# Kernel optimization log

Hardware: AMD Instinct MI355X
Metric: run time of the kernel (lower is better)

## Reference

```python
import jax, jax.numpy as jnp
import numpy as np

WS = 7          # window size
NUM_HEADS = 12

def _relative_position_index(ws):
    # Same construction as the torch module; pure numpy constants.
    coords = np.stack(np.meshgrid(np.arange(ws), np.arange(ws), indexing='ij'))  # [2, ws, ws]
    flat = coords.reshape(2, -1)                                                 # [2, N]
    rel = flat[:, :, None] - flat[:, None, :]                                    # [2, N, N]
    rel = rel.transpose(1, 2, 0).copy()                                          # [N, N, 2]
    rel[:, :, 0] += ws - 1
    rel[:, :, 1] += ws - 1
    rel[:, :, 0] *= 2 * ws - 1
    return rel.sum(-1)                                                           # [N, N] int

REL_IDX = jnp.asarray(_relative_position_index(WS))

def setup_inputs() -> dict:
    key = jax.random.key(0)
    ks = jax.random.split(key, 7)
    C, H = 384, NUM_HEADS
    B_, N = 2048, WS * WS
    return {
        "x": jax.random.normal(ks[0], (B_, N, C), jnp.float32),
        "mask": jax.random.normal(ks[1], (64, N, N), jnp.float32),
        "qkv_w": jax.random.normal(ks[2], (3 * C, C), jnp.float32) * 0.02,
        "qkv_b": jax.random.normal(ks[3], (3 * C,), jnp.float32) * 0.02,
        "proj_w": jax.random.normal(ks[4], (C, C), jnp.float32) * 0.02,
        "proj_b": jax.random.normal(ks[5], (C,), jnp.float32) * 0.02,
        "rpb_table": jax.random.normal(ks[6], ((2 * WS - 1) ** 2, H), jnp.float32) * 0.02,
    }

def reference(x, mask, qkv_w, qkv_b, proj_w, proj_b, rpb_table):
    B_, N, C = x.shape
    H = NUM_HEADS
    hd = C // H
    scale = hd ** (-0.5)

    qkv = x @ qkv_w.T + qkv_b                                   # [B_, N, 3C]
    qkv = qkv.reshape(B_, N, 3, H, hd).transpose(2, 0, 3, 1, 4)  # [3, B_, H, N, hd]
    q, k, v = qkv[0], qkv[1], qkv[2]

    attn = jnp.einsum('bhnd,bhmd->bhnm', q * scale, k)          # [B_, H, N, N]

    bias = rpb_table[REL_IDX]                                   # [N, N, H]
    attn = attn + bias.transpose(2, 0, 1)[None]                 # + [1, H, N, N]

    nw = mask.shape[0]
    attn = attn.reshape(B_ // nw, nw, H, N, N) + mask[None, :, None]
    attn = attn.reshape(B_, H, N, N)
    attn = jax.nn.softmax(attn, axis=-1)

    out = jnp.einsum('bhnm,bhmd->bhnd', attn, v)                # [B_, H, N, hd]
    out = out.transpose(0, 2, 1, 3).reshape(B_, N, C)
    return out @ proj_w.T + proj_b
```

## Files before the change

### kernel.cpp

```cpp
#include <hip/hip_runtime.h>
#include <stdint.h>
#include <stddef.h>

#define BWIN 2048
#define NTOK 49
#define CDIM 384
#define HNUM 12
#define HD   32
#define MTOT (BWIN * NTOK)
#define LOG2E 1.4426950408889634f
#define QSCALE ((float)(0.17677669529663687 * 1.4426950408889634))

typedef __attribute__((ext_vector_type(8))) short short8;
typedef __attribute__((ext_vector_type(4))) float floatx4;

__device__ __forceinline__ unsigned short f2bf(float f) {
    union { float f; unsigned u; } v; v.f = f;
    unsigned u = v.u;
    u = u + 0x7fffu + ((u >> 16) & 1u);
    return (unsigned short)(u >> 16);
}

__device__ __forceinline__ void gload16(const void* g, void* l) {
    __builtin_amdgcn_global_load_lds(
        (const __attribute__((address_space(1))) void*)g,
        (__attribute__((address_space(3))) void*)l, 16, 0, 0);
}

#define XBLK  18816
#define WQBLK 216
#define WPBLK 72
__global__ __launch_bounds__(256) void convert_kernel(
    const float* __restrict__ x, const float* __restrict__ wq,
    const float* __restrict__ wp, unsigned short* __restrict__ xbf,
    unsigned short* __restrict__ wqbf, unsigned short* __restrict__ wpbf)
{
    int bid = blockIdx.x;
    const float* src; unsigned short* dst; size_t base;
    if (bid < XBLK)              { src = x;  dst = xbf;  base = (size_t)bid * 2048; }
    else if (bid < XBLK + WQBLK) { src = wq; dst = wqbf; base = (size_t)(bid - XBLK) * 2048; }
    else                         { src = wp; dst = wpbf; base = (size_t)(bid - XBLK - WQBLK) * 2048; }
    const size_t i = base + (size_t)threadIdx.x * 8;
    float4 a = *(const float4*)(src + i);
    float4 b = *(const float4*)(src + i + 4);
    unsigned short o[8] = {f2bf(a.x), f2bf(a.y), f2bf(a.z), f2bf(a.w),
                           f2bf(b.x), f2bf(b.y), f2bf(b.z), f2bf(b.w)};
    *(uint4*)(dst + i) = *(uint4*)o;
}

__global__ __launch_bounds__(256) void bias_kernel(
    const float* __restrict__ mask, const float* __restrict__ rpb,
    float* __restrict__ cb)
{
    const int bm = blockIdx.x, h = blockIdx.y;
    const int tid = threadIdx.x;
    const int w = tid >> 6, lane = tid & 63;
    const int cg = lane & 15, rg = lane >> 4;
    const int rbase = 16 * w + (rg << 2);
    const float* mk = mask + (size_t)bm * (NTOK * NTOK);
    float o[16];
    #pragma unroll
    for (int j = 0; j < 4; ++j) {
        const int col = 16 * j + cg;
        const bool vc = col < NTOK;
        int yj = 0, xj = 0;
        if (vc) { yj = col / 7; xj = col - yj * 7; }
        #pragma unroll
        for (int r = 0; r < 4; ++r) {
            const int row = rbase + r;
            float v = -1e30f;
            if (vc && row < NTOK) {
                const int yi = row / 7, xi = row - yi * 7;
                const int rel = (yi - yj + 6) * 13 + (xi - xj + 6);
                v = (rpb[rel * HNUM + h] + mk[row * NTOK + col]) * LOG2E;
            }
            o[4 * j + r] = v;
        }
    }
    float* dst = cb + ((size_t)bm * HNUM + h) * 4096 + (size_t)tid * 16;
    #pragma unroll
    for (int j = 0; j < 4; ++j)
        *(float4*)(dst + 4 * j) = *(const float4*)(o + 4 * j);
}

__global__ __launch_bounds__(256) void qkv_kernel(
    const unsigned short* __restrict__ a, const unsigned short* __restrict__ b,
    const float* __restrict__ bias, unsigned short* __restrict__ outq)
{
    __shared__ __align__(16) unsigned short lA[3][128 * 32];
    __shared__ __align__(16) unsigned short lB[3][128 * 32];

    const int tid = threadIdx.x;
    const int lane = tid & 63, w = tid >> 6;

    const int bid = blockIdx.x;
    const int wg = (bid & 7) * 882 + (bid >> 3);
    const int tN = (wg % 9) * 128;
    const int tM = (wg / 9) * 128;

    const int X = (lane << 4) ^ (((lane >> 3) & 7) << 4);
    const int srow = (w << 5) + (X >> 6);
    const int scol = (X & 63) >> 1;
    const unsigned short* gA = a + (size_t)(tM + srow) * CDIM + scol;
    const unsigned short* gB = b + (size_t)(tN + srow) * CDIM + scol;

    const int wm = (w & 1) << 6, wn = (w >> 1) << 6;
    const int cg = lane & 15, rg = lane >> 4;

    floatx4 acc[4][4];
    #pragma unroll
    for (int i = 0; i < 4; ++i)
        #pragma unroll
        for (int j = 0; j < 4; ++j) acc[i][j] = (floatx4){0.f, 0.f, 0.f, 0.f};

    int offA[4], offB[4];
    #pragma unroll
    for (int i = 0; i < 4; ++i) {
        const int rowA = wm + 16 * i + cg;
        const int sA = (rowA << 6) + (rg << 4);
        offA[i] = sA ^ (((sA >> 7) & 7) << 4);
        const int rowB = wn + 16 * i + cg;
        const int sB = (rowB << 6) + (rg << 4);
        offB[i] = sB ^ (((sB >> 7) & 7) << 4);
    }

    #define STAGE_Q(BUF, K0) do {                                          \
        unsigned short* _lAb = &lA[(BUF)][w << 10];                        \
        unsigned short* _lBb = &lB[(BUF)][w << 10];                        \
        gload16(gA + (K0),              _lAb);                             \
        gload16(gA + (K0) + 16 * CDIM,  _lAb + 512);                       \
        gload16(gB + (K0),              _lBb);                             \
        gload16(gB + (K0) + 16 * CDIM,  _lBb + 512);                       \
    } while (0)

    STAGE_Q(0, 0);
    STAGE_Q(1, 32);

    #pragma unroll
    for (int t = 0; t < 12; ++t) {
        if (t < 11) asm volatile("s_waitcnt vmcnt(4)" ::: "memory");
        else        asm volatile("s_waitcnt vmcnt(0)" ::: "memory");
        __builtin_amdgcn_s_barrier();
        __builtin_amdgcn_sched_barrier(0);

        const int bufb = (t % 3) * (128 * 32 * 2);
        short8 af[4], bfr[4];
        #pragma unroll
        for (int i = 0; i < 4; ++i)
            af[i] = *(const short8*)((const char*)lA + bufb + offA[i]);
        #pragma unroll
        for (int j = 0; j < 4; ++j)
            bfr[j] = *(const short8*)((const char*)lB + bufb + offB[j]);

        if (t < 10) STAGE_Q((t + 2) % 3, (t + 2) * 32);

        __builtin_amdgcn_s_setprio(1);
        #pragma unroll
        for (int i = 0; i < 4; ++i)
            #pragma unroll
            for (int j = 0; j < 4; ++j)
                acc[i][j] = __builtin_amdgcn_mfma_f32_16x16x32_bf16(af[i], bfr[j], acc[i][j], 0, 0, 0);
        __builtin_amdgcn_s_setprio(0);
    }
    #undef STAGE_Q

    const int r0 = tM + wm + (rg << 2);
    float bv[4], sc[4];
    size_t cjo[4];
    #pragma unroll
    for (int j = 0; j < 4; ++j) {
        const int col = tN + wn + 16 * j + cg;
        bv[j] = bias[col];
        const int which = col / CDIM;
        const int rem = col - which * CDIM;
        const int h = rem >> 5, d = rem & 31;
        sc[j] = (which == 0) ? QSCALE : 1.0f;
        cjo[j] = (size_t)which * (BWIN * HNUM * NTOK * HD)
               + (size_t)h * (NTOK * HD) + d;
    }
    #pragma unroll
    for (int i = 0; i < 4; ++i) {
        #pragma unroll
        for (int r = 0; r < 4; ++r) {
            const int row = r0 + 16 * i + r;
            const int bb = row / NTOK;
            const int n = row - bb * NTOK;
            const size_t ro = (size_t)bb * (HNUM * NTOK * HD) + (size_t)n * HD;
            #pragma unroll
            for (int j = 0; j < 4; ++j)
                outq[cjo[j] + ro] = f2bf((acc[i][j][r] + bv[j]) * sc[j]);
        }
    }
}

__global__ __launch_bounds__(256) void attn_kernel(
    const unsigned short* __restrict__ qkv, const float* __restrict__ cb,
    unsigned short* __restrict__ outa)
{
    __shared__ __align__(16) unsigned short lq[64][40];
    __shared__ __align__(16) unsigned short lk[64][40];
    __shared__ __align__(16) unsigned short lvt[32][72];
    __shared__ __align__(16) unsigned short lp[64][72];

    const int b = blockIdx.x, h = blockIdx.y;
    const int tid = threadIdx.x;
    const size_t WHICH = (size_t)BWIN * HNUM * NTOK * HD;
    const size_t base = ((size_t)b * HNUM + h) * (NTOK * HD);

    const float* cbp = cb + ((size_t)(b & 63) * HNUM + h) * 4096 + (size_t)tid * 16;
    floatx4 z[4];
    #pragma unroll
    for (int j = 0; j < 4; ++j) z[j] = *(const floatx4*)(cbp + 4 * j);

    for (int e = tid; e < 1152; e += 256)
        ((unsigned*)&lvt[0][0])[e] = 0u;
    if (tid < 240) {
        const int r = 49 + (tid >> 4), c = (tid & 15) * 2;
        *(unsigned*)&lq[r][c] = 0u;
        *(unsigned*)&lk[r][c] = 0u;
    }
    uint4 vreg;
    if (tid < 196) {
        const int n = tid >> 2, d = (tid & 3) * 8;
        *(uint4*)&lq[n][d] = *(const uint4*)(qkv + base + tid * 8);
        *(uint4*)&lk[n][d] = *(const uint4*)(qkv + base + WHICH + tid * 8);
        vreg = *(const uint4*)(qkv + base + 2 * WHICH + tid * 8);
    }
    __syncthreads();

    if (tid < 196) {
        const int n = tid >> 2, d0 = (tid & 3) * 8;
        const unsigned short* vp = (const unsigned short*)&vreg;
        #pragma unroll
        for (int jj = 0; jj < 8; ++jj)
            lvt[d0 + jj][n] = vp[jj];
    }

    const int w = tid >> 6, lane = tid & 63;
    const int cg = lane & 15;
    const int rg = lane >> 4;
    const int rbase = 16 * w + rg * 4;

    short8 aq = *(const short8*)&lq[16 * w + cg][rg * 8];
    floatx4 s[4];
    #pragma unroll
    for (int j = 0; j < 4; ++j) {
        short8 bk = *(const short8*)&lk[16 * j + cg][rg * 8];
        s[j] = __builtin_amdgcn_mfma_f32_16x16x32_bf16(aq, bk, z[j], 0, 0, 0);
    }

    float l[4] = {0.f, 0.f, 0.f, 0.f};
    #pragma unroll
    for (int j = 0; j < 4; ++j) {
        const int col = 16 * j + cg;
        #pragma unroll
        for (int r = 0; r < 4; ++r) {
            const float e = exp2f(s[j][r]);
            l[r] += e;
            lp[rbase + r][col] = f2bf(e);
        }
    }
    #pragma unroll
    for (int st = 1; st < 16; st <<= 1) {
        #pragma unroll
        for (int r = 0; r < 4; ++r) l[r] += __shfl_xor(l[r], st);
    }
    float linv[4];
    #pragma unroll
    for (int r = 0; r < 4; ++r) linv[r] = 1.f / l[r];
    __syncthreads();

    #pragma unroll
    for (int n = 0; n < 2; ++n) {
        floatx4 o = {0, 0, 0, 0};
        #pragma unroll
        for (int kk = 0; kk < 2; ++kk) {
            short8 ap = *(const short8*)&lp[16 * w + cg][kk * 32 + rg * 8];
            short8 bv = *(const short8*)&lvt[16 * n + cg][kk * 32 + rg * 8];
            o = __builtin_amdgcn_mfma_f32_16x16x32_bf16(ap, bv, o, 0, 0, 0);
        }
        #pragma unroll
        for (int r = 0; r < 4; ++r) {
            const int row = rbase + r;
            if (row < NTOK)
                outa[((size_t)b * NTOK + row) * CDIM + h * HD + n * 16 + cg] =
                    f2bf(o[r] * linv[r]);
        }
    }
}

__global__ __launch_bounds__(256) void proj_kernel(
    const unsigned short* __restrict__ a, const unsigned short* __restrict__ b,
    const float* __restrict__ bias, float* __restrict__ out)
{
    __shared__ __align__(16) unsigned short lA[3][128 * 32];
    __shared__ __align__(16) unsigned short lB[3][128 * 32];

    const int tid = threadIdx.x;
    const int lane = tid & 63, w = tid >> 6;

    const int bid = blockIdx.x;
    const int wg = (bid & 7) * 294 + (bid >> 3);
    const int tN = (wg % 3) * 128;
    const int tM = (wg / 3) * 128;

    const int X = (lane << 4) ^ (((lane >> 3) & 7) << 4);
    const int srow = (w << 5) + (X >> 6);
    const int scol = (X & 63) >> 1;
    const unsigned short* gA = a + (size_t)(tM + srow) * CDIM + scol;
    const unsigned short* gB = b + (size_t)(tN + srow) * CDIM + scol;

    const int wm = (w & 1) << 6, wn = (w >> 1) << 6;
    const int cg = lane & 15, rg = lane >> 4;

    floatx4 acc[4][4];
    #pragma unroll
    for (int i = 0; i < 4; ++i)
        #pragma unroll
        for (int j = 0; j < 4; ++j) acc[i][j] = (floatx4){0.f, 0.f, 0.f, 0.f};

    int offA[4], offB[4];
    #pragma unroll
    for (int i = 0; i < 4; ++i) {
        const int rowA = wm + 16 * i + cg;
        const int sA = (rowA << 6) + (rg << 4);
        offA[i] = sA ^ (((sA >> 7) & 7) << 4);
        const int rowB = wn + 16 * i + cg;
        const int sB = (rowB << 6) + (rg << 4);
        offB[i] = sB ^ (((sB >> 7) & 7) << 4);
    }

    #define STAGE_P(BUF, K0) do {                                          \
        unsigned short* _lAb = &lA[(BUF)][w << 10];                        \
        unsigned short* _lBb = &lB[(BUF)][w << 10];                        \
        gload16(gA + (K0),              _lAb);                             \
        gload16(gA + (K0) + 16 * CDIM,  _lAb + 512);                       \
        gload16(gB + (K0),              _lBb);                             \
        gload16(gB + (K0) + 16 * CDIM,  _lBb + 512);                       \
    } while (0)

    STAGE_P(0, 0);
    STAGE_P(1, 32);

    #pragma unroll
    for (int t = 0; t < 12; ++t) {
        if (t < 11) asm volatile("s_waitcnt vmcnt(4)" ::: "memory");
        else        asm volatile("s_waitcnt vmcnt(0)" ::: "memory");
        __builtin_amdgcn_s_barrier();
        __builtin_amdgcn_sched_barrier(0);

        const int bufb = (t % 3) * (128 * 32 * 2);
        short8 af[4], bfr[4];
        #pragma unroll
        for (int i = 0; i < 4; ++i)
            af[i] = *(const short8*)((const char*)lA + bufb + offA[i]);
        #pragma unroll
        for (int j = 0; j < 4; ++j)
            bfr[j] = *(const short8*)((const char*)lB + bufb + offB[j]);

        if (t < 10) STAGE_P((t + 2) % 3, (t + 2) * 32);

        __builtin_amdgcn_s_setprio(1);
        #pragma unroll
        for (int i = 0; i < 4; ++i)
            #pragma unroll
            for (int j = 0; j < 4; ++j)
                acc[i][j] = __builtin_amdgcn_mfma_f32_16x16x32_bf16(af[i], bfr[j], acc[i][j], 0, 0, 0);
        __builtin_amdgcn_s_setprio(0);
    }
    #undef STAGE_P

    const int r0 = tM + wm + (rg << 2);
    #pragma unroll
    for (int j = 0; j < 4; ++j) {
        const int col = tN + wn + 16 * j + cg;
        const float bv = bias[col];
        #pragma unroll
        for (int i = 0; i < 4; ++i) {
            #pragma unroll
            for (int r = 0; r < 4; ++r) {
                const int row = r0 + 16 * i + r;
                out[(size_t)row * CDIM + col] = acc[i][j][r] + bv;
            }
        }
    }
}

extern "C" void kernel_launch(void* const* d_in, const int* in_sizes, int n_in,
                              void* d_out, int out_size, void* d_ws, size_t ws_size,
                              hipStream_t stream) {
    const float* x      = (const float*)d_in[0];
    const float* mask   = (const float*)d_in[1];
    const float* qkv_w  = (const float*)d_in[2];
    const float* qkv_b  = (const float*)d_in[3];
    const float* proj_w = (const float*)d_in[4];
    const float* proj_b = (const float*)d_in[5];
    const float* rpb    = (const float*)d_in[6];
    float* out = (float*)d_out;

    unsigned short* ws_qkv  = (unsigned short*)d_ws;
    unsigned short* xbf     = ws_qkv + (size_t)3 * BWIN * HNUM * NTOK * HD;
    unsigned short* ws_attn = xbf;
    unsigned short* wqbf    = xbf + (size_t)MTOT * CDIM;
    unsigned short* wpbf    = wqbf + (size_t)3 * CDIM * CDIM;
    float* cbias            = (float*)(wpbf + (size_t)CDIM * CDIM);

    convert_kernel<<<XBLK + WQBLK + WPBLK, 256, 0, stream>>>(x, qkv_w, proj_w, xbf, wqbf, wpbf);
    bias_kernel<<<dim3(64, HNUM), 256, 0, stream>>>(mask, rpb, cbias);
    qkv_kernel<<<7056, 256, 0, stream>>>(xbf, wqbf, qkv_b, ws_qkv);
    attn_kernel<<<dim3(BWIN, HNUM), 256, 0, stream>>>(ws_qkv, cbias, ws_attn);
    proj_kernel<<<2352, 256, 0, stream>>>(ws_attn, wpbf, proj_b, out);
}
```

Before: 575.9 us.

## Load GEMM A operand directly from global into registers, bypassing LDS

In both the QKV and projection GEMMs, the A-operand tile is no longer staged through shared memory. Each wave instead loads its own MFMA A fragments straight from global memory into double-buffered registers, one K-step ahead. Only B still goes through the triple-buffered LDS pipeline. This halves LDS traffic and shared-memory footprint, which could allow more resident blocks. In exchange, A loads become per-lane 16-byte strided global reads that are reused less across waves, and they add register pressure and rely on vmcnt ordering with the mixed load types.

```diff
diff --git a/kernel.cpp b/kernel.cpp
--- a/kernel.cpp
+++ b/kernel.cpp
@@ -87,7 +87,6 @@
     const unsigned short* __restrict__ a, const unsigned short* __restrict__ b,
     const float* __restrict__ bias, unsigned short* __restrict__ outq)
 {
-    __shared__ __align__(16) unsigned short lA[3][128 * 32];
     __shared__ __align__(16) unsigned short lB[3][128 * 32];
 
     const int tid = threadIdx.x;
@@ -101,68 +100,74 @@
     const int X = (lane << 4) ^ (((lane >> 3) & 7) << 4);
     const int srow = (w << 5) + (X >> 6);
     const int scol = (X & 63) >> 1;
-    const unsigned short* gA = a + (size_t)(tM + srow) * CDIM + scol;
     const unsigned short* gB = b + (size_t)(tN + srow) * CDIM + scol;
 
     const int wm = (w & 1) << 6, wn = (w >> 1) << 6;
     const int cg = lane & 15, rg = lane >> 4;
 
+    const unsigned short* gAf = a + (size_t)(tM + wm + cg) * CDIM + (rg << 3);
+
     floatx4 acc[4][4];
     #pragma unroll
     for (int i = 0; i < 4; ++i)
         #pragma unroll
         for (int j = 0; j < 4; ++j) acc[i][j] = (floatx4){0.f, 0.f, 0.f, 0.f};
 
-    int offA[4], offB[4];
-    #pragma unroll
-    for (int i = 0; i < 4; ++i) {
-        const int rowA = wm + 16 * i + cg;
-        const int sA = (rowA << 6) + (rg << 4);
-        offA[i] = sA ^ (((sA >> 7) & 7) << 4);
-        const int rowB = wn + 16 * i + cg;
+    int offB[4];
+    #pragma unroll
+    for (int j = 0; j < 4; ++j) {
+        const int rowB = wn + 16 * j + cg;
         const int sB = (rowB << 6) + (rg << 4);
-        offB[i] = sB ^ (((sB >> 7) & 7) << 4);
-    }
-
-    #define STAGE_Q(BUF, K0) do {                                          \
-        unsigned short* _lAb = &lA[(BUF)][w << 10];                        \
+        offB[j] = sB ^ (((sB >> 7) & 7) << 4);
+    }
+
+    #define STAGE_B(BUF, K0) do {                                          \
         unsigned short* _lBb = &lB[(BUF)][w << 10];                        \
-        gload16(gA + (K0),              _lAb);                             \
-        gload16(gA + (K0) + 16 * CDIM,  _lAb + 512);                       \
         gload16(gB + (K0),              _lBb);                             \
         gload16(gB + (K0) + 16 * CDIM,  _lBb + 512);                       \
     } while (0)
-
-    STAGE_Q(0, 0);
-    STAGE_Q(1, 32);
+    #define LOAD_A(DST, K0) do {                                           \
+        DST[0] = *(const short8*)(gAf + (K0));                             \
+        DST[1] = *(const short8*)(gAf + 16 * CDIM + (K0));                 \
+        DST[2] = *(const short8*)(gAf + 32 * CDIM + (K0));                 \
+        DST[3] = *(const short8*)(gAf + 48 * CDIM + (K0));                 \
+    } while (0)
+
+    short8 aA0[4], aA1[4];
+    STAGE_B(0, 0);
+    LOAD_A(aA0, 0);
+    STAGE_B(1, 32);
 
     #pragma unroll
     for (int t = 0; t < 12; ++t) {
-        if (t < 11) asm volatile("s_waitcnt vmcnt(4)" ::: "memory");
+        if (t < 11) asm volatile("s_waitcnt vmcnt(2)" ::: "memory");
         else        asm volatile("s_waitcnt vmcnt(0)" ::: "memory");
         __builtin_amdgcn_s_barrier();
         __builtin_amdgcn_sched_barrier(0);
 
-        const int bufb = (t % 3) * (128 * 32 * 2);
-        short8 af[4], bfr[4];
-        #pragma unroll
-        for (int i = 0; i < 4; ++i)
-            af[i] = *(const short8*)((const char*)lA + bufb + offA[i]);
+        const int bufb = (t % 3) * 8192;
+        short8 bfr[4];
         #pragma unroll
         for (int j = 0; j < 4; ++j)
             bfr[j] = *(const short8*)((const char*)lB + bufb + offB[j]);
 
-        if (t < 10) STAGE_Q((t + 2) % 3, (t + 2) * 32);
+        if (t < 11) {
+            if (t & 1) LOAD_A(aA0, (t + 1) * 32);
+            else       LOAD_A(aA1, (t + 1) * 32);
+        }
+        if (t < 10) STAGE_B((t + 2) % 3, (t + 2) * 32);
 
         __builtin_amdgcn_s_setprio(1);
         #pragma unroll
         for (int i = 0; i < 4; ++i)
             #pragma unroll
             for (int j = 0; j < 4; ++j)
-                acc[i][j] = __builtin_amdgcn_mfma_f32_16x16x32_bf16(af[i], bfr[j], acc[i][j], 0, 0, 0);
+                acc[i][j] = __builtin_amdgcn_mfma_f32_16x16x32_bf16(
+                    (t & 1) ? aA1[i] : aA0[i], bfr[j], acc[i][j], 0, 0, 0);
         __builtin_amdgcn_s_setprio(0);
     }
-    #undef STAGE_Q
+    #undef STAGE_B
+    #undef LOAD_A
 
     const int r0 = tM + wm + (rg << 2);
     float bv[4], sc[4];
@@ -293,7 +298,6 @@
     const unsigned short* __restrict__ a, const unsigned short* __restrict__ b,
     const float* __restrict__ bias, float* __restrict__ out)
 {
-    __shared__ __align__(16) unsigned short lA[3][128 * 32];
     __shared__ __align__(16) unsigned short lB[3][128 * 32];
 
     const int tid = threadIdx.x;
@@ -307,68 +311,74 @@
     const int X = (lane << 4) ^ (((lane >> 3) & 7) << 4);
     const int srow = (w << 5) + (X >> 6);
     const int scol = (X & 63) >> 1;
-    const unsigned short* gA = a + (size_t)(tM + srow) * CDIM + scol;
     const unsigned short* gB = b + (size_t)(tN + srow) * CDIM + scol;
 
     const int wm = (w & 1) << 6, wn = (w >> 1) << 6;
     const int cg = lane & 15, rg = lane >> 4;
 
+    const unsigned short* gAf = a + (size_t)(tM + wm + cg) * CDIM + (rg << 3);
+
     floatx4 acc[4][4];
     #pragma unroll
     for (int i = 0; i < 4; ++i)
         #pragma unroll
         for (int j = 0; j < 4; ++j) acc[i][j] = (floatx4){0.f, 0.f, 0.f, 0.f};
 
-    int offA[4], offB[4];
-    #pragma unroll
-    for (int i = 0; i < 4; ++i) {
-        const int rowA = wm + 16 * i + cg;
-        const int sA = (rowA << 6) + (rg << 4);
-        offA[i] = sA ^ (((sA >> 7) & 7) << 4);
-        const int rowB = wn + 16 * i + cg;
+    int offB[4];
+    #pragma unroll
+    for (int j = 0; j < 4; ++j) {
+        const int rowB = wn + 16 * j + cg;
         const int sB = (rowB << 6) + (rg << 4);
-        offB[i] = sB ^ (((sB >> 7) & 7) << 4);
-    }
-
-    #define STAGE_P(BUF, K0) do {                                          \
-        unsigned short* _lAb = &lA[(BUF)][w << 10];                        \
+        offB[j] = sB ^ (((sB >> 7) & 7) << 4);
+    }
+
+    #define STAGE_B(BUF, K0) do {                                          \
         unsigned short* _lBb = &lB[(BUF)][w << 10];                        \
-        gload16(gA + (K0),              _lAb);                             \
-        gload16(gA + (K0) + 16 * CDIM,  _lAb + 512);                       \
         gload16(gB + (K0),              _lBb);                             \
         gload16(gB + (K0) + 16 * CDIM,  _lBb + 512);                       \
     } while (0)
-
-    STAGE_P(0, 0);
-    STAGE_P(1, 32);
+    #define LOAD_A(DST, K0) do {                                           \
+        DST[0] = *(const short8*)(gAf + (K0));                             \
+        DST[1] = *(const short8*)(gAf + 16 * CDIM + (K0));                 \
+        DST[2] = *(const short8*)(gAf + 32 * CDIM + (K0));                 \
+        DST[3] = *(const short8*)(gAf + 48 * CDIM + (K0));                 \
+    } while (0)
+
+    short8 aA0[4], aA1[4];
+    STAGE_B(0, 0);
+    LOAD_A(aA0, 0);
+    STAGE_B(1, 32);
 
     #pragma unroll
     for (int t = 0; t < 12; ++t) {
-        if (t < 11) asm volatile("s_waitcnt vmcnt(4)" ::: "memory");
+        if (t < 11) asm volatile("s_waitcnt vmcnt(2)" ::: "memory");
         else        asm volatile("s_waitcnt vmcnt(0)" ::: "memory");
         __builtin_amdgcn_s_barrier();
         __builtin_amdgcn_sched_barrier(0);
 
-        const int bufb = (t % 3) * (128 * 32 * 2);
-        short8 af[4], bfr[4];
-        #pragma unroll
-        for (int i = 0; i < 4; ++i)
-            af[i] = *(const short8*)((const char*)lA + bufb + offA[i]);
+        const int bufb = (t % 3) * 8192;
+        short8 bfr[4];
         #pragma unroll
         for (int j = 0; j < 4; ++j)
             bfr[j] = *(const short8*)((const char*)lB + bufb + offB[j]);
 
-        if (t < 10) STAGE_P((t + 2) % 3, (t + 2) * 32);
+        if (t < 11) {
+            if (t & 1) LOAD_A(aA0, (t + 1) * 32);
+            else       LOAD_A(aA1, (t + 1) * 32);
+        }
+        if (t < 10) STAGE_B((t + 2) % 3, (t + 2) * 32);
 
         __builtin_amdgcn_s_setprio(1);
         #pragma unroll
         for (int i = 0; i < 4; ++i)
             #pragma unroll
             for (int j = 0; j < 4; ++j)
-                acc[i][j] = __builtin_amdgcn_mfma_f32_16x16x32_bf16(af[i], bfr[j], acc[i][j], 0, 0, 0);
+                acc[i][j] = __builtin_amdgcn_mfma_f32_16x16x32_bf16(
+                    (t & 1) ? aA1[i] : aA0[i], bfr[j], acc[i][j], 0, 0, 0);
         __builtin_amdgcn_s_setprio(0);
     }
-    #undef STAGE_P
+    #undef STAGE_B
+    #undef LOAD_A
 
     const int r0 = tM + wm + (rg << 2);
     #pragma unroll
```

After: 669.0 us. 1.16x slower.

## Fuse fp32-to-bf16 conversion of x into the QKV GEMM load path

Applied to the files above, without the earlier changes.

Removes the separate pass that converts x to bf16 in global memory. The QKV GEMM now reads fp32 x straight into registers, packs it to bf16 with v_cvt_pk_bf16_f32, and writes it to a double-buffered, swizzled LDS tile, while B keeps its async global-to-LDS triple buffer. This saves a full write and reread of the bf16 copy of x. In exchange, the GEMM reads twice as many bytes for A, and each of the 9 N-tiles rereads the fp32 A. It also adds register pressure and an lgkmcnt wait before every barrier.

```diff
diff --git a/kernel.cpp b/kernel.cpp
--- a/kernel.cpp
+++ b/kernel.cpp
@@ -21,25 +21,28 @@
     return (unsigned short)(u >> 16);
 }
 
+__device__ __forceinline__ unsigned pkbf(float lo, float hi) {
+    unsigned r;
+    asm volatile("v_cvt_pk_bf16_f32 %0, %1, %2" : "=v"(r) : "v"(lo), "v"(hi));
+    return r;
+}
+
 __device__ __forceinline__ void gload16(const void* g, void* l) {
     __builtin_amdgcn_global_load_lds(
         (const __attribute__((address_space(1))) void*)g,
         (__attribute__((address_space(3))) void*)l, 16, 0, 0);
 }
 
-#define XBLK  18816
 #define WQBLK 216
 #define WPBLK 72
 __global__ __launch_bounds__(256) void convert_kernel(
-    const float* __restrict__ x, const float* __restrict__ wq,
-    const float* __restrict__ wp, unsigned short* __restrict__ xbf,
+    const float* __restrict__ wq, const float* __restrict__ wp,
     unsigned short* __restrict__ wqbf, unsigned short* __restrict__ wpbf)
 {
     int bid = blockIdx.x;
     const float* src; unsigned short* dst; size_t base;
-    if (bid < XBLK)              { src = x;  dst = xbf;  base = (size_t)bid * 2048; }
-    else if (bid < XBLK + WQBLK) { src = wq; dst = wqbf; base = (size_t)(bid - XBLK) * 2048; }
-    else                         { src = wp; dst = wpbf; base = (size_t)(bid - XBLK - WQBLK) * 2048; }
+    if (bid < WQBLK) { src = wq; dst = wqbf; base = (size_t)bid * 2048; }
+    else             { src = wp; dst = wpbf; base = (size_t)(bid - WQBLK) * 2048; }
     const size_t i = base + (size_t)threadIdx.x * 8;
     float4 a = *(const float4*)(src + i);
     float4 b = *(const float4*)(src + i + 4);
@@ -84,10 +87,10 @@
 }
 
 __global__ __launch_bounds__(256) void qkv_kernel(
-    const unsigned short* __restrict__ a, const unsigned short* __restrict__ b,
+    const float* __restrict__ a, const unsigned short* __restrict__ b,
     const float* __restrict__ bias, unsigned short* __restrict__ outq)
 {
-    __shared__ __align__(16) unsigned short lA[3][128 * 32];
+    __shared__ __align__(16) unsigned short lA[2][128 * 32];
     __shared__ __align__(16) unsigned short lB[3][128 * 32];
 
     const int tid = threadIdx.x;
@@ -101,8 +104,14 @@
     const int X = (lane << 4) ^ (((lane >> 3) & 7) << 4);
     const int srow = (w << 5) + (X >> 6);
     const int scol = (X & 63) >> 1;
-    const unsigned short* gA = a + (size_t)(tM + srow) * CDIM + scol;
     const unsigned short* gB = b + (size_t)(tN + srow) * CDIM + scol;
+
+    const int arow = (w << 5) + (lane >> 1);
+    const float* gAx = a + (size_t)(tM + arow) * CDIM + ((lane & 1) << 4);
+    const int d0lin = (arow << 6) + ((lane & 1) << 5);
+    const int dX = ((lane >> 2) & 7) << 4;
+    const int d0 = d0lin ^ dX;
+    const int d1 = (d0lin + 16) ^ dX;
 
     const int wm = (w & 1) << 6, wn = (w >> 1) << 6;
     const int cg = lane & 15, rg = lane >> 4;
@@ -124,35 +133,60 @@
         offB[i] = sB ^ (((sB >> 7) & 7) << 4);
     }
 
-    #define STAGE_Q(BUF, K0) do {                                          \
-        unsigned short* _lAb = &lA[(BUF)][w << 10];                        \
+    #define STAGE_B(BUF, K0) do {                                          \
         unsigned short* _lBb = &lB[(BUF)][w << 10];                        \
-        gload16(gA + (K0),              _lAb);                             \
-        gload16(gA + (K0) + 16 * CDIM,  _lAb + 512);                       \
         gload16(gB + (K0),              _lBb);                             \
         gload16(gB + (K0) + 16 * CDIM,  _lBb + 512);                       \
     } while (0)
-
-    STAGE_Q(0, 0);
-    STAGE_Q(1, 32);
+    #define ALOAD(SET, K0) do {                                            \
+        SET[0] = *(const float4*)(gAx + (K0));                             \
+        SET[1] = *(const float4*)(gAx + (K0) + 4);                         \
+        SET[2] = *(const float4*)(gAx + (K0) + 8);                         \
+        SET[3] = *(const float4*)(gAx + (K0) + 12);                        \
+    } while (0)
+    #define AWRITE(SET, BUF) do {                                          \
+        uint4 q0, q1;                                                      \
+        q0.x = pkbf(SET[0].x, SET[0].y); q0.y = pkbf(SET[0].z, SET[0].w);  \
+        q0.z = pkbf(SET[1].x, SET[1].y); q0.w = pkbf(SET[1].z, SET[1].w);  \
+        q1.x = pkbf(SET[2].x, SET[2].y); q1.y = pkbf(SET[2].z, SET[2].w);  \
+        q1.z = pkbf(SET[3].x, SET[3].y); q1.w = pkbf(SET[3].z, SET[3].w);  \
+        *(uint4*)((char*)&lA[(BUF)][0] + d0) = q0;                         \
+        *(uint4*)((char*)&lA[(BUF)][0] + d1) = q1;                         \
+    } while (0)
+
+    float4 rA0[4], rA1[4];
+    ALOAD(rA0, 0);
+    STAGE_B(0, 0);
+    ALOAD(rA1, 32);
+    STAGE_B(1, 32);
+    asm volatile("s_waitcnt vmcnt(8)" ::: "memory");
+    AWRITE(rA0, 0);
 
     #pragma unroll
     for (int t = 0; t < 12; ++t) {
-        if (t < 11) asm volatile("s_waitcnt vmcnt(4)" ::: "memory");
+        if (t < 11) asm volatile("s_waitcnt vmcnt(2)" ::: "memory");
         else        asm volatile("s_waitcnt vmcnt(0)" ::: "memory");
+        asm volatile("s_waitcnt lgkmcnt(0)" ::: "memory");
         __builtin_amdgcn_s_barrier();
         __builtin_amdgcn_sched_barrier(0);
 
-        const int bufb = (t % 3) * (128 * 32 * 2);
         short8 af[4], bfr[4];
         #pragma unroll
         for (int i = 0; i < 4; ++i)
-            af[i] = *(const short8*)((const char*)lA + bufb + offA[i]);
+            af[i] = *(const short8*)((const char*)&lA[t & 1][0] + offA[i]);
         #pragma unroll
         for (int j = 0; j < 4; ++j)
-            bfr[j] = *(const short8*)((const char*)lB + bufb + offB[j]);
-
-        if (t < 10) STAGE_Q((t + 2) % 3, (t + 2) * 32);
+            bfr[j] = *(const short8*)((const char*)&lB[t % 3][0] + offB[j]);
+
+        if (t <= 9) {
+            if (t & 1) ALOAD(rA1, (t + 2) * 32);
+            else       ALOAD(rA0, (t + 2) * 32);
+        }
+        if (t <= 10) {
+            if (t & 1) AWRITE(rA0, (t + 1) & 1);
+            else       AWRITE(rA1, (t + 1) & 1);
+        }
+        if (t <= 9) STAGE_B((t + 2) % 3, (t + 2) * 32);
 
         __builtin_amdgcn_s_setprio(1);
         #pragma unroll
@@ -162,7 +196,9 @@
                 acc[i][j] = __builtin_amdgcn_mfma_f32_16x16x32_bf16(af[i], bfr[j], acc[i][j], 0, 0, 0);
         __builtin_amdgcn_s_setprio(0);
     }
-    #undef STAGE_Q
+    #undef STAGE_B
+    #undef ALOAD
+    #undef AWRITE
 
     const int r0 = tM + wm + (rg << 2);
     float bv[4], sc[4];
@@ -349,7 +385,7 @@
         __builtin_amdgcn_s_barrier();
         __builtin_amdgcn_sched_barrier(0);
 
-        const int bufb = (t % 3) * (128 * 32 * 2);
+        const int bufb = (t % 3) * 8192;
         short8 af[4], bfr[4];
         #pragma unroll
         for (int i = 0; i < 4; ++i)
@@ -399,15 +435,14 @@
     float* out = (float*)d_out;
 
     unsigned short* ws_qkv  = (unsigned short*)d_ws;
-    unsigned short* xbf     = ws_qkv + (size_t)3 * BWIN * HNUM * NTOK * HD;
-    unsigned short* ws_attn = xbf;
-    unsigned short* wqbf    = xbf + (size_t)MTOT * CDIM;
+    unsigned short* ws_attn = ws_qkv + (size_t)3 * BWIN * HNUM * NTOK * HD;
+    unsigned short* wqbf    = ws_attn + (size_t)MTOT * CDIM;
     unsigned short* wpbf    = wqbf + (size_t)3 * CDIM * CDIM;
     float* cbias            = (float*)(wpbf + (size_t)CDIM * CDIM);
 
-    convert_kernel<<<XBLK + WQBLK + WPBLK, 256, 0, stream>>>(x, qkv_w, proj_w, xbf, wqbf, wpbf);
+    convert_kernel<<<WQBLK + WPBLK, 256, 0, stream>>>(qkv_w, proj_w, wqbf, wpbf);
     bias_kernel<<<dim3(64, HNUM), 256, 0, stream>>>(mask, rpb, cbias);
-    qkv_kernel<<<7056, 256, 0, stream>>>(xbf, wqbf, qkv_b, ws_qkv);
+    qkv_kernel<<<7056, 256, 0, stream>>>(x, wqbf, qkv_b, ws_qkv);
     attn_kernel<<<dim3(BWIN, HNUM), 256, 0, stream>>>(ws_qkv, cbias, ws_attn);
     proj_kernel<<<2352, 256, 0, stream>>>(ws_attn, wpbf, proj_b, out);
 }
```

Result: slower. 622.6 us (+8.1%).

## Loop over heads in attention block and prefetch next head's Q/K/V

Applied to the files above, without the earlier changes.

The attention kernel now launches one block per window instead of one per (window, head) and loops over all 12 heads inside the block. While the current head's softmax and PV run, it prefetches the next head's Q/K/V and bias tile into registers, hiding global load latency. The bufb constant edits in the GEMMs are cosmetic. The trade-off is a 12x smaller grid with serialized heads and extra barriers per head, which may reduce parallelism and latency hiding across blocks.

```diff
diff --git a/kernel.cpp b/kernel.cpp
--- a/kernel.cpp
+++ b/kernel.cpp
@@ -143,7 +143,7 @@
         __builtin_amdgcn_s_barrier();
         __builtin_amdgcn_sched_barrier(0);
 
-        const int bufb = (t % 3) * (128 * 32 * 2);
+        const int bufb = (t % 3) * 8192;
         short8 af[4], bfr[4];
         #pragma unroll
         for (int i = 0; i < 4; ++i)
@@ -202,15 +202,13 @@
     __shared__ __align__(16) unsigned short lvt[32][72];
     __shared__ __align__(16) unsigned short lp[64][72];
 
-    const int b = blockIdx.x, h = blockIdx.y;
+    const int b = blockIdx.x;
     const int tid = threadIdx.x;
     const size_t WHICH = (size_t)BWIN * HNUM * NTOK * HD;
-    const size_t base = ((size_t)b * HNUM + h) * (NTOK * HD);
-
-    const float* cbp = cb + ((size_t)(b & 63) * HNUM + h) * 4096 + (size_t)tid * 16;
-    floatx4 z[4];
-    #pragma unroll
-    for (int j = 0; j < 4; ++j) z[j] = *(const floatx4*)(cbp + 4 * j);
+    const size_t hstep = (size_t)NTOK * HD;
+    const size_t base0 = (size_t)b * HNUM * hstep;
+
+    const float* cbb = cb + (size_t)(b & 63) * HNUM * 4096 + (size_t)tid * 16;
 
     for (int e = tid; e < 1152; e += 256)
         ((unsigned*)&lvt[0][0])[e] = 0u;
@@ -219,72 +217,112 @@
         *(unsigned*)&lq[r][c] = 0u;
         *(unsigned*)&lk[r][c] = 0u;
     }
-    uint4 vreg;
+
+    const int w = tid >> 6, lane = tid & 63;
+    const int cg = lane & 15, rg = lane >> 4;
+    const int rbase = 16 * w + (rg << 2);
+    const int vn = tid >> 2, vd = (tid & 3) * 8;
+
+    uint4 vq, vk, vv;
     if (tid < 196) {
-        const int n = tid >> 2, d = (tid & 3) * 8;
-        *(uint4*)&lq[n][d] = *(const uint4*)(qkv + base + tid * 8);
-        *(uint4*)&lk[n][d] = *(const uint4*)(qkv + base + WHICH + tid * 8);
-        vreg = *(const uint4*)(qkv + base + 2 * WHICH + tid * 8);
+        vq = *(const uint4*)(qkv + base0 + tid * 8);
+        vk = *(const uint4*)(qkv + base0 + WHICH + tid * 8);
+        vv = *(const uint4*)(qkv + base0 + 2 * WHICH + tid * 8);
+    }
+    floatx4 z[4];
+    #pragma unroll
+    for (int j = 0; j < 4; ++j) z[j] = *(const floatx4*)(cbb + 4 * j);
+    if (tid < 196) {
+        *(uint4*)&lq[vn][vd] = vq;
+        *(uint4*)&lk[vn][vd] = vk;
+        const unsigned short* vp = (const unsigned short*)&vv;
+        #pragma unroll
+        for (int jj = 0; jj < 8; ++jj)
+            lvt[vd + jj][vn] = vp[jj];
     }
     __syncthreads();
 
-    if (tid < 196) {
-        const int n = tid >> 2, d0 = (tid & 3) * 8;
-        const unsigned short* vp = (const unsigned short*)&vreg;
-        #pragma unroll
-        for (int jj = 0; jj < 8; ++jj)
-            lvt[d0 + jj][n] = vp[jj];
-    }
-
-    const int w = tid >> 6, lane = tid & 63;
-    const int cg = lane & 15;
-    const int rg = lane >> 4;
-    const int rbase = 16 * w + rg * 4;
-
-    short8 aq = *(const short8*)&lq[16 * w + cg][rg * 8];
-    floatx4 s[4];
-    #pragma unroll
-    for (int j = 0; j < 4; ++j) {
-        short8 bk = *(const short8*)&lk[16 * j + cg][rg * 8];
-        s[j] = __builtin_amdgcn_mfma_f32_16x16x32_bf16(aq, bk, z[j], 0, 0, 0);
-    }
-
-    float l[4] = {0.f, 0.f, 0.f, 0.f};
-    #pragma unroll
-    for (int j = 0; j < 4; ++j) {
-        const int col = 16 * j + cg;
-        #pragma unroll
-        for (int r = 0; r < 4; ++r) {
-            const float e = exp2f(s[j][r]);
-            l[r] += e;
-            lp[rbase + r][col] = f2bf(e);
-        }
-    }
-    #pragma unroll
-    for (int st = 1; st < 16; st <<= 1) {
-        #pragma unroll
-        for (int r = 0; r < 4; ++r) l[r] += __shfl_xor(l[r], st);
-    }
-    float linv[4];
-    #pragma unroll
-    for (int r = 0; r < 4; ++r) linv[r] = 1.f / l[r];
-    __syncthreads();
-
-    #pragma unroll
-    for (int n = 0; n < 2; ++n) {
-        floatx4 o = {0, 0, 0, 0};
-        #pragma unroll
-        for (int kk = 0; kk < 2; ++kk) {
-            short8 ap = *(const short8*)&lp[16 * w + cg][kk * 32 + rg * 8];
-            short8 bv = *(const short8*)&lvt[16 * n + cg][kk * 32 + rg * 8];
-            o = __builtin_amdgcn_mfma_f32_16x16x32_bf16(ap, bv, o, 0, 0, 0);
-        }
-        #pragma unroll
-        for (int r = 0; r < 4; ++r) {
-            const int row = rbase + r;
-            if (row < NTOK)
-                outa[((size_t)b * NTOK + row) * CDIM + h * HD + n * 16 + cg] =
-                    f2bf(o[r] * linv[r]);
+    for (int h = 0; h < HNUM; ++h) {
+        short8 aq = *(const short8*)&lq[16 * w + cg][rg * 8];
+        floatx4 s[4];
+        #pragma unroll
+        for (int j = 0; j < 4; ++j) {
+            short8 bk = *(const short8*)&lk[16 * j + cg][rg * 8];
+            s[j] = __builtin_amdgcn_mfma_f32_16x16x32_bf16(aq, bk, z[j], 0, 0, 0);
+        }
+
+        floatx4 zn[4];
+        if (h < HNUM - 1) {
+            const size_t baseh = base0 + (size_t)(h + 1) * hstep;
+            if (tid < 196) {
+                vq = *(const uint4*)(qkv + baseh + tid * 8);
+                vk = *(const uint4*)(qkv + baseh + WHICH + tid * 8);
+                vv = *(const uint4*)(qkv + baseh + 2 * WHICH + tid * 8);
+            }
+            const float* cbn = cbb + (size_t)(h + 1) * 4096;
+            #pragma unroll
+            for (int j = 0; j < 4; ++j) zn[j] = *(const floatx4*)(cbn + 4 * j);
+        }
+
+        float l[4] = {0.f, 0.f, 0.f, 0.f};
+        #pragma unroll
+        for (int j = 0; j < 4; ++j) {
+            const int col = 16 * j + cg;
+            #pragma unroll
+            for (int r = 0; r < 4; ++r) {
+                const float e = exp2f(s[j][r]);
+                l[r] += e;
+                lp[rbase + r][col] = f2bf(e);
+            }
+        }
+        #pragma unroll
+        for (int st = 1; st < 16; st <<= 1) {
+            #pragma unroll
+            for (int r = 0; r < 4; ++r) l[r] += __shfl_xor(l[r], st);
+        }
+        float linv[4];
+        #pragma unroll
+        for (int r = 0; r < 4; ++r) linv[r] = 1.f / l[r];
+
+        asm volatile("s_waitcnt lgkmcnt(0)" ::: "memory");
+        __builtin_amdgcn_s_barrier();
+        __builtin_amdgcn_sched_barrier(0);
+
+        #pragma unroll
+        for (int n = 0; n < 2; ++n) {
+            floatx4 o = {0, 0, 0, 0};
+            #pragma unroll
+            for (int kk = 0; kk < 2; ++kk) {
+                short8 ap = *(const short8*)&lp[16 * w + cg][kk * 32 + rg * 8];
+                short8 bvv = *(const short8*)&lvt[16 * n + cg][kk * 32 + rg * 8];
+                o = __builtin_amdgcn_mfma_f32_16x16x32_bf16(ap, bvv, o, 0, 0, 0);
+            }
+            #pragma unroll
+            for (int r = 0; r < 4; ++r) {
+                const int row = rbase + r;
+                if (row < NTOK)
+                    outa[((size_t)b * NTOK + row) * CDIM + h * HD + n * 16 + cg] =
+                        f2bf(o[r] * linv[r]);
+            }
+        }
+
+        __builtin_amdgcn_s_barrier();
+        __builtin_amdgcn_sched_barrier(0);
+
+        if (h < HNUM - 1) {
+            if (tid < 196) {
+                *(uint4*)&lq[vn][vd] = vq;
+                *(uint4*)&lk[vn][vd] = vk;
+                const unsigned short* vp = (const unsigned short*)&vv;
+                #pragma unroll
+                for (int jj = 0; jj < 8; ++jj)
+                    lvt[vd + jj][vn] = vp[jj];
+            }
+            #pragma unroll
+            for (int j = 0; j < 4; ++j) z[j] = zn[j];
+            asm volatile("s_waitcnt lgkmcnt(0)" ::: "memory");
+            __builtin_amdgcn_s_barrier();
+            __builtin_amdgcn_sched_barrier(0);
         }
     }
 }
@@ -349,7 +387,7 @@
         __builtin_amdgcn_s_barrier();
         __builtin_amdgcn_sched_barrier(0);
 
-        const int bufb = (t % 3) * (128 * 32 * 2);
+        const int bufb = (t % 3) * 8192;
         short8 af[4], bfr[4];
         #pragma unroll
         for (int i = 0; i < 4; ++i)
@@ -408,6 +446,6 @@
     convert_kernel<<<XBLK + WQBLK + WPBLK, 256, 0, stream>>>(x, qkv_w, proj_w, xbf, wqbf, wpbf);
     bias_kernel<<<dim3(64, HNUM), 256, 0, stream>>>(mask, rpb, cbias);
     qkv_kernel<<<7056, 256, 0, stream>>>(xbf, wqbf, qkv_b, ws_qkv);
-    attn_kernel<<<dim3(BWIN, HNUM), 256, 0, stream>>>(ws_qkv, cbias, ws_attn);
+    attn_kernel<<<BWIN, 256, 0, stream>>>(ws_qkv, cbias, ws_attn);
     proj_kernel<<<2352, 256, 0, stream>>>(ws_attn, wpbf, proj_b, out);
 }
```

Result: slower. 588.5 us (+2.2%).
